# Kernel optimization log

Hardware: AMD Instinct MI355X
Metric: run time of the kernel (lower is better)

## Reference

```python
import jax, jax.numpy as jnp
import numpy as np

# Dimensions matching init_kwargs
O = 4096   # out_features
I = 4096   # in_features
R = 32     # svd_rank
G = 64     # n_groups
GS = I // G  # group_size = 64
NBITS = 4
NUM_BYTES = O * I * NBITS // 8


def setup_inputs() -> dict:
    key = jax.random.key(0)
    ks = jax.random.split(key, 7)
    return {
        "x": jax.random.normal(ks[0], (1, 4096, I), dtype=jnp.float32),
        # bit-packed int4 weights, two nibbles per byte (stored as int32 holding 0..255)
        "w_packed": jax.random.randint(ks[1], (NUM_BYTES,), 0, 256, dtype=jnp.int32),
        "svd_up": jax.random.normal(ks[2], (O, R), dtype=jnp.float32) * 0.02,
        "svd_down": jax.random.normal(ks[3], (R, I), dtype=jnp.float32) * 0.02,
        "scale": jax.random.uniform(ks[4], (O, G, 1), dtype=jnp.float32, minval=0.001, maxval=0.02),
        "zero_point": jax.random.uniform(ks[5], (O, G, 1), dtype=jnp.float32, minval=0.0, maxval=15.0),
        "bias": jax.random.normal(ks[6], (O,), dtype=jnp.float32) * 0.01,
    }


def _dequantize(w_packed, svd_up, svd_down, scale, zero_point):
    # Unpack two 4-bit values per byte (low nibble first).
    low = w_packed & 0xF
    high = (w_packed >> 4) & 0xF
    w_q = jnp.stack([low, high], axis=-1).reshape(O, G, GS).astype(jnp.float32)
    # Per-group affine dequant: (q - zero) * scale, then SVD low-rank correction.
    W = ((w_q - zero_point) * scale).reshape(O, I)
    return W + svd_up @ svd_down  # [O, I]


def reference(x, w_packed, svd_up, svd_down, scale, zero_point, bias):
    # forward_int8 path (tokens > 16, int8_matmul=True)
    W_f = _dequantize(w_packed, svd_up, svd_down, scale, zero_point).T  # [I, O]
    xm = x.reshape(-1, I)  # [N, I]
    # Dynamic per-row activation quant
    scale_x = jnp.max(jnp.abs(xm), axis=1, keepdims=True) / 127.0  # [N, 1]
    x_q = jnp.clip(jnp.round(xm / scale_x), -128, 127).astype(jnp.int8)
    # Dynamic per-column weight quant
    scale_w = jnp.max(jnp.abs(W_f), axis=0, keepdims=True) / 127.0  # [1, O]
    W_q = jnp.clip(jnp.round(W_f / scale_w), -128, 127).astype(jnp.int8)
    # int8 GEMM with int32 accumulation, then dequant scales + bias
    acc = jnp.matmul(x_q.astype(jnp.int32), W_q.astype(jnp.int32))  # [N, O] int32
    out = acc.astype(jnp.float32) * scale_x * scale_w + bias
    return out.reshape(*x.shape[:-1], O)
```

## Files before the change

### kernel.cpp

```cpp
#include <hip/hip_runtime.h>
#include <cstdint>
#include <cstddef>

#define I_DIM 4096
#define O_DIM 4096
#define RNK 32
#define NGRP 64
#define N_TOK 4096

typedef int v4i  __attribute__((ext_vector_type(4)));
typedef int v16i __attribute__((ext_vector_type(16)));

__device__ __forceinline__ int clamp_i8(float v) {
    int q = (int)rintf(v);
    q = q < -128 ? -128 : q;
    q = q > 127 ? 127 : q;
    return q;
}

#define BO 4

__global__ __launch_bounds__(256, 4) void quant_w_kernel(
    const int* __restrict__ w_packed, const float* __restrict__ svd_up,
    const float* __restrict__ svd_down, const float* __restrict__ scale,
    const float* __restrict__ zp, char* __restrict__ w_q,
    float* __restrict__ scale_w)
{
    __shared__ float s_sc[BO][NGRP];
    __shared__ float s_zp[BO][NGRP];
    __shared__ float s_red[BO][4];
    __shared__ float s_sw[BO];

    const int tid = threadIdx.x;
    const int o0 = blockIdx.x * BO;

    for (int t = tid; t < BO * NGRP; t += 256) {
        s_sc[t >> 6][t & 63] = scale[(size_t)(o0 + (t >> 6)) * NGRP + (t & 63)];
        s_zp[t >> 6][t & 63] = zp[(size_t)(o0 + (t >> 6)) * NGRP + (t & 63)];
    }
    __syncthreads();

    float W[4][BO][4];
    float vmax[BO];
#pragma unroll
    for (int ro = 0; ro < BO; ro++) vmax[ro] = 0.0f;

#pragma unroll
    for (int jq = 0; jq < 4; jq++) {
        const int q = tid + 256 * jq;
        const int i = 4 * q;
        const int g = q >> 4;

#pragma unroll
        for (int ro = 0; ro < BO; ro++) {
            const int2 b2 = *(const int2*)&w_packed[(size_t)(o0 + ro) * (I_DIM / 2) + 2 * q];
            const float sc = s_sc[ro][g], z = s_zp[ro][g];
            W[jq][ro][0] = ((float)(b2.x & 0xF) - z) * sc;
            W[jq][ro][1] = ((float)((b2.x >> 4) & 0xF) - z) * sc;
            W[jq][ro][2] = ((float)(b2.y & 0xF) - z) * sc;
            W[jq][ro][3] = ((float)((b2.y >> 4) & 0xF) - z) * sc;
        }

#pragma unroll 4
        for (int r = 0; r < RNK; r++) {
            const float4 d = *(const float4*)&svd_down[(size_t)r * I_DIM + i];
#pragma unroll
            for (int ro = 0; ro < BO; ro++) {
                const float u = svd_up[(size_t)(o0 + ro) * RNK + r];
                W[jq][ro][0] += u * d.x;
                W[jq][ro][1] += u * d.y;
                W[jq][ro][2] += u * d.z;
                W[jq][ro][3] += u * d.w;
            }
        }

#pragma unroll
        for (int ro = 0; ro < BO; ro++) {
            vmax[ro] = fmaxf(vmax[ro],
                fmaxf(fmaxf(fabsf(W[jq][ro][0]), fabsf(W[jq][ro][1])),
                      fmaxf(fabsf(W[jq][ro][2]), fabsf(W[jq][ro][3]))));
        }
    }

    const int lane = tid & 63, wv = tid >> 6;
#pragma unroll
    for (int ro = 0; ro < BO; ro++) {
        float m = vmax[ro];
        for (int off = 32; off > 0; off >>= 1)
            m = fmaxf(m, __shfl_down(m, off, 64));
        if (lane == 0) s_red[ro][wv] = m;
    }
    __syncthreads();
    if (tid < BO) {
        const float m = fmaxf(fmaxf(s_red[tid][0], s_red[tid][1]),
                              fmaxf(s_red[tid][2], s_red[tid][3]));
        const float sw = m / 127.0f;
        scale_w[o0 + tid] = sw;
        s_sw[tid] = sw;
    }
    __syncthreads();

    float inv[BO];
#pragma unroll
    for (int ro = 0; ro < BO; ro++) inv[ro] = 1.0f / s_sw[ro];

#pragma unroll
    for (int jq = 0; jq < 4; jq++) {
        const int q = tid + 256 * jq;
#pragma unroll
        for (int ro = 0; ro < BO; ro++) {
            const int q0 = clamp_i8(W[jq][ro][0] * inv[ro]);
            const int q1 = clamp_i8(W[jq][ro][1] * inv[ro]);
            const int q2 = clamp_i8(W[jq][ro][2] * inv[ro]);
            const int q3 = clamp_i8(W[jq][ro][3] * inv[ro]);
            ((int*)w_q)[(size_t)(o0 + ro) * (I_DIM / 4) + q] =
                (q0 & 0xFF) | ((q1 & 0xFF) << 8) | ((q2 & 0xFF) << 16) | ((q3 & 0xFF) << 24);
        }
    }
}

__global__ __launch_bounds__(256) void quant_x_kernel(
    const float* __restrict__ x, char* __restrict__ x_q,
    float* __restrict__ scale_x)
{
    const int n = blockIdx.x;
    const int tid = threadIdx.x;
    const float4* xr = (const float4*)(x + (size_t)n * I_DIM);
    float4 v[4];
    float m = 0.0f;
#pragma unroll
    for (int j = 0; j < 4; j++) {
        v[j] = xr[tid + 256 * j];
        m = fmaxf(m, fmaxf(fmaxf(fabsf(v[j].x), fabsf(v[j].y)),
                           fmaxf(fabsf(v[j].z), fabsf(v[j].w))));
    }
    __shared__ float s_red[4];
    __shared__ float s_sx;
    for (int off = 32; off > 0; off >>= 1)
        m = fmaxf(m, __shfl_down(m, off, 64));
    if ((tid & 63) == 0) s_red[tid >> 6] = m;
    __syncthreads();
    if (tid == 0) {
        const float mm = fmaxf(fmaxf(s_red[0], s_red[1]),
                               fmaxf(s_red[2], s_red[3]));
        const float sx = mm / 127.0f;
        scale_x[n] = sx;
        s_sx = sx;
    }
    __syncthreads();
    const float sx = s_sx;
    int* outw = (int*)(x_q + (size_t)n * I_DIM);
#pragma unroll
    for (int j = 0; j < 4; j++) {
        const int q0 = clamp_i8(v[j].x / sx);
        const int q1 = clamp_i8(v[j].y / sx);
        const int q2 = clamp_i8(v[j].z / sx);
        const int q3 = clamp_i8(v[j].w / sx);
        outw[tid + 256 * j] =
            (q0 & 0xFF) | ((q1 & 0xFF) << 8) | ((q2 & 0xFF) << 16) | ((q3 & 0xFF) << 24);
    }
}

#define BM 128
#define BN 128
#define BK 128

__global__ __launch_bounds__(256) void gemm_i8_kernel(
    const char* __restrict__ x_q, const char* __restrict__ w_q,
    const float* __restrict__ scale_x, const float* __restrict__ scale_w,
    const float* __restrict__ bias, float* __restrict__ out)
{
    __shared__ v4i As4[BM * BK / 16];
    __shared__ v4i Bs4[BN * BK / 16];
    char* As = (char*)As4;
    char* Bs = (char*)Bs4;

    const int tid = threadIdx.x;
    const int id = blockIdx.x;
    const int xcd = id & 7;
    const int s_lin = id >> 3;
    const int bm0 = (s_lin & 31) * BM;
    const int bn0 = (xcd * 4 + (s_lin >> 5)) * BN;

    const int lane = tid & 63, wv = tid >> 6;
    const int wm = wv & 1, wn = wv >> 1;
    const int l31 = lane & 31, h = lane >> 5;

    v16i acc[2][2];
#pragma unroll
    for (int mt = 0; mt < 2; mt++)
#pragma unroll
        for (int nt = 0; nt < 2; nt++)
            acc[mt][nt] = (v16i)(0);

    for (int kk = 0; kk < I_DIM / BK; kk++) {
        const int k0 = kk * BK;
#pragma unroll
        for (int j = 0; j < 4; j++) {
            const int c = tid + 256 * j;
            const int row = c >> 3;
            const int kc = (c & 7) ^ (row & 7);
            const char* ga = x_q + (size_t)(bm0 + row) * I_DIM + k0 + kc * 16;
            __builtin_amdgcn_global_load_lds(
                (const __attribute__((address_space(1))) unsigned int*)ga,
                (__attribute__((address_space(3))) unsigned int*)(As + c * 16),
                16, 0, 0);
            const char* gb = w_q + (size_t)(bn0 + row) * I_DIM + k0 + kc * 16;
            __builtin_amdgcn_global_load_lds(
                (const __attribute__((address_space(1))) unsigned int*)gb,
                (__attribute__((address_space(3))) unsigned int*)(Bs + c * 16),
                16, 0, 0);
        }
        __syncthreads();
#pragma unroll
        for (int s = 0; s < 4; s++) {
            v4i af[2], bf[2];
#pragma unroll
            for (int mt = 0; mt < 2; mt++) {
                const int row = wm * 64 + mt * 32 + l31;
                const int kc = (s * 2 + h) ^ (row & 7);
                af[mt] = *(const v4i*)(As + row * BK + kc * 16);
            }
#pragma unroll
            for (int nt = 0; nt < 2; nt++) {
                const int row = wn * 64 + nt * 32 + l31;
                const int kc = (s * 2 + h) ^ (row & 7);
                bf[nt] = *(const v4i*)(Bs + row * BK + kc * 16);
            }
#pragma unroll
            for (int mt = 0; mt < 2; mt++)
#pragma unroll
                for (int nt = 0; nt < 2; nt++)
                    acc[mt][nt] = __builtin_amdgcn_mfma_i32_32x32x32_i8(
                        af[mt], bf[nt], acc[mt][nt], 0, 0, 0);
        }
        __syncthreads();
    }

#pragma unroll
    for (int mt = 0; mt < 2; mt++) {
        const int rbase = bm0 + wm * 64 + mt * 32 + 4 * h;
        float sx[16];
#pragma unroll
        for (int reg = 0; reg < 16; reg++)
            sx[reg] = scale_x[rbase + (reg & 3) + 8 * (reg >> 2)];
#pragma unroll
        for (int nt = 0; nt < 2; nt++) {
            const int oc = bn0 + wn * 64 + nt * 32 + l31;
            const float sw = scale_w[oc];
            const float bs = bias[oc];
#pragma unroll
            for (int reg = 0; reg < 16; reg++) {
                const int rr = rbase + (reg & 3) + 8 * (reg >> 2);
                out[(size_t)rr * O_DIM + oc] =
                    (float)acc[mt][nt][reg] * sx[reg] * sw + bs;
            }
        }
    }
}

extern "C" void kernel_launch(void* const* d_in, const int* in_sizes, int n_in,
                              void* d_out, int out_size, void* d_ws, size_t ws_size,
                              hipStream_t stream) {
    const float* x        = (const float*)d_in[0];
    const int*   w_packed = (const int*)d_in[1];
    const float* svd_up   = (const float*)d_in[2];
    const float* svd_down = (const float*)d_in[3];
    const float* scale    = (const float*)d_in[4];
    const float* zp       = (const float*)d_in[5];
    const float* bias     = (const float*)d_in[6];
    float* out = (float*)d_out;

    char* ws = (char*)d_ws;
    char*  w_q     = ws;
    char*  x_q     = ws + ((size_t)16 << 20);
    float* scale_w = (float*)(ws + ((size_t)32 << 20));
    float* scale_x = (float*)(ws + ((size_t)32 << 20) + 16384);

    quant_w_kernel<<<O_DIM / BO, 256, 0, stream>>>(w_packed, svd_up, svd_down,
                                                   scale, zp, w_q, scale_w);
    quant_x_kernel<<<N_TOK, 256, 0, stream>>>(x, x_q, scale_x);
    gemm_i8_kernel<<<(N_TOK / BM) * (O_DIM / BN), 256, 0, stream>>>(
        x_q, w_q, scale_x, scale_w, bias, out);
}
```

Measured before the change: 261.3 us.

## Merge quant kernels and rewrite int8 GEMM with 256x256 triple-buffered pipeline

```diff
diff --git a/kernel.cpp b/kernel.cpp
--- a/kernel.cpp
+++ b/kernel.cpp
@@ -19,12 +19,13 @@
 }
 
 #define BO 4
-
-__global__ __launch_bounds__(256, 4) void quant_w_kernel(
+#define W_BLOCKS (O_DIM / BO)
+
+__device__ __forceinline__ void quant_w_body(
     const int* __restrict__ w_packed, const float* __restrict__ svd_up,
     const float* __restrict__ svd_down, const float* __restrict__ scale,
     const float* __restrict__ zp, char* __restrict__ w_q,
-    float* __restrict__ scale_w)
+    float* __restrict__ scale_w, int blk)
 {
     __shared__ float s_sc[BO][NGRP];
     __shared__ float s_zp[BO][NGRP];
@@ -32,7 +33,7 @@
     __shared__ float s_sw[BO];
 
     const int tid = threadIdx.x;
-    const int o0 = blockIdx.x * BO;
+    const int o0 = blk * BO;
 
     for (int t = tid; t < BO * NGRP; t += 256) {
         s_sc[t >> 6][t & 63] = scale[(size_t)(o0 + (t >> 6)) * NGRP + (t & 63)];
@@ -41,16 +42,11 @@
     __syncthreads();
 
     float W[4][BO][4];
-    float vmax[BO];
-#pragma unroll
-    for (int ro = 0; ro < BO; ro++) vmax[ro] = 0.0f;
 
 #pragma unroll
     for (int jq = 0; jq < 4; jq++) {
         const int q = tid + 256 * jq;
-        const int i = 4 * q;
         const int g = q >> 4;
-
 #pragma unroll
         for (int ro = 0; ro < BO; ro++) {
             const int2 b2 = *(const int2*)&w_packed[(size_t)(o0 + ro) * (I_DIM / 2) + 2 * q];
@@ -60,27 +56,39 @@
             W[jq][ro][2] = ((float)(b2.y & 0xF) - z) * sc;
             W[jq][ro][3] = ((float)((b2.y >> 4) & 0xF) - z) * sc;
         }
-
-#pragma unroll 4
-        for (int r = 0; r < RNK; r++) {
-            const float4 d = *(const float4*)&svd_down[(size_t)r * I_DIM + i];
+    }
+
+#pragma unroll 2
+    for (int r = 0; r < RNK; r++) {
+        float u[BO];
+#pragma unroll
+        for (int ro = 0; ro < BO; ro++)
+            u[ro] = svd_up[(size_t)(o0 + ro) * RNK + r];
+        float4 d[4];
+#pragma unroll
+        for (int jq = 0; jq < 4; jq++)
+            d[jq] = *(const float4*)&svd_down[(size_t)r * I_DIM + 4 * (tid + 256 * jq)];
+#pragma unroll
+        for (int jq = 0; jq < 4; jq++)
 #pragma unroll
             for (int ro = 0; ro < BO; ro++) {
-                const float u = svd_up[(size_t)(o0 + ro) * RNK + r];
-                W[jq][ro][0] += u * d.x;
-                W[jq][ro][1] += u * d.y;
-                W[jq][ro][2] += u * d.z;
-                W[jq][ro][3] += u * d.w;
+                W[jq][ro][0] += u[ro] * d[jq].x;
+                W[jq][ro][1] += u[ro] * d[jq].y;
+                W[jq][ro][2] += u[ro] * d[jq].z;
+                W[jq][ro][3] += u[ro] * d[jq].w;
             }
-        }
-
-#pragma unroll
-        for (int ro = 0; ro < BO; ro++) {
+    }
+
+    float vmax[BO];
+#pragma unroll
+    for (int ro = 0; ro < BO; ro++) vmax[ro] = 0.0f;
+#pragma unroll
+    for (int jq = 0; jq < 4; jq++)
+#pragma unroll
+        for (int ro = 0; ro < BO; ro++)
             vmax[ro] = fmaxf(vmax[ro],
                 fmaxf(fmaxf(fabsf(W[jq][ro][0]), fabsf(W[jq][ro][1])),
                       fmaxf(fabsf(W[jq][ro][2]), fabsf(W[jq][ro][3]))));
-        }
-    }
 
     const int lane = tid & 63, wv = tid >> 6;
 #pragma unroll
@@ -119,11 +127,10 @@
     }
 }
 
-__global__ __launch_bounds__(256) void quant_x_kernel(
+__device__ __forceinline__ void quant_x_body(
     const float* __restrict__ x, char* __restrict__ x_q,
-    float* __restrict__ scale_x)
-{
-    const int n = blockIdx.x;
+    float* __restrict__ scale_x, int n)
+{
     const int tid = threadIdx.x;
     const float4* xr = (const float4*)(x + (size_t)n * I_DIM);
     float4 v[4];
@@ -161,85 +168,128 @@
     }
 }
 
-#define BM 128
-#define BN 128
-#define BK 128
-
-__global__ __launch_bounds__(256) void gemm_i8_kernel(
+__global__ __launch_bounds__(256, 4) void prep_kernel(
+    const int* __restrict__ w_packed, const float* __restrict__ svd_up,
+    const float* __restrict__ svd_down, const float* __restrict__ scale,
+    const float* __restrict__ zp, char* __restrict__ w_q,
+    float* __restrict__ scale_w,
+    const float* __restrict__ x, char* __restrict__ x_q,
+    float* __restrict__ scale_x)
+{
+    if (blockIdx.x < W_BLOCKS)
+        quant_w_body(w_packed, svd_up, svd_down, scale, zp, w_q, scale_w, blockIdx.x);
+    else
+        quant_x_body(x, x_q, scale_x, blockIdx.x - W_BLOCKS);
+}
+
+#define TBM 256
+#define TBN 256
+#define TBK 64
+#define NKT (I_DIM / TBK)
+
+__device__ __forceinline__ void stage_tile(const char* __restrict__ src, int row0,
+                                           int t, char* lds_mat, int tid)
+{
+#pragma unroll
+    for (int uu = 0; uu < 2; uu++) {
+        const int c = tid + uu * 512;
+        const int row = c >> 2;
+        const int kc = (c & 3) ^ ((row >> 1) & 3);
+        const char* g = src + (size_t)(row0 + row) * I_DIM + t * TBK + kc * 16;
+        __builtin_amdgcn_global_load_lds(
+            (const __attribute__((address_space(1))) unsigned int*)g,
+            (__attribute__((address_space(3))) unsigned int*)(lds_mat + c * 16),
+            16, 0, 0);
+    }
+}
+
+#define READ_FRAGS(P) do {                                                  \
+    _Pragma("unroll")                                                       \
+    for (int mt = 0; mt < 4; mt++) {                                        \
+        const int row = wm * 128 + mt * 32 + l31;                           \
+        const int kc = ((P) * 2 + h) ^ ((row >> 1) & 3);                    \
+        af[mt] = *(const v4i*)(Ac + row * TBK + kc * 16);                   \
+    }                                                                       \
+    _Pragma("unroll")                                                       \
+    for (int nt = 0; nt < 2; nt++) {                                        \
+        const int row = wn * 64 + nt * 32 + l31;                            \
+        const int kc = ((P) * 2 + h) ^ ((row >> 1) & 3);                    \
+        bf[nt] = *(const v4i*)(Bc + row * TBK + kc * 16);                   \
+    }                                                                       \
+} while (0)
+
+#define MFMA_CLUSTER() do {                                                 \
+    __builtin_amdgcn_s_setprio(1);                                          \
+    _Pragma("unroll")                                                       \
+    for (int mt = 0; mt < 4; mt++)                                          \
+        _Pragma("unroll")                                                   \
+        for (int nt = 0; nt < 2; nt++)                                      \
+            acc[mt][nt] = __builtin_amdgcn_mfma_i32_32x32x32_i8(            \
+                af[mt], bf[nt], acc[mt][nt], 0, 0, 0);                      \
+    __builtin_amdgcn_s_setprio(0);                                          \
+} while (0)
+
+__global__ __launch_bounds__(512, 2) void gemm_i8_kernel(
     const char* __restrict__ x_q, const char* __restrict__ w_q,
     const float* __restrict__ scale_x, const float* __restrict__ scale_w,
     const float* __restrict__ bias, float* __restrict__ out)
 {
-    __shared__ v4i As4[BM * BK / 16];
-    __shared__ v4i Bs4[BN * BK / 16];
-    char* As = (char*)As4;
-    char* Bs = (char*)Bs4;
+    __shared__ v4i smem4[3 * 2 * 1024];
+    char* lds = (char*)smem4;
 
     const int tid = threadIdx.x;
     const int id = blockIdx.x;
     const int xcd = id & 7;
-    const int s_lin = id >> 3;
-    const int bm0 = (s_lin & 31) * BM;
-    const int bn0 = (xcd * 4 + (s_lin >> 5)) * BN;
+    const int s = id >> 3;
+    const int bm0 = (s & 15) * TBM;
+    const int bn0 = (xcd * 2 + (s >> 4)) * TBN;
 
     const int lane = tid & 63, wv = tid >> 6;
-    const int wm = wv & 1, wn = wv >> 1;
+    const int wm = wv >> 2, wn = wv & 3;
     const int l31 = lane & 31, h = lane >> 5;
 
-    v16i acc[2][2];
-#pragma unroll
-    for (int mt = 0; mt < 2; mt++)
+    v16i acc[4][2];
+#pragma unroll
+    for (int mt = 0; mt < 4; mt++)
 #pragma unroll
         for (int nt = 0; nt < 2; nt++)
             acc[mt][nt] = (v16i)(0);
 
-    for (int kk = 0; kk < I_DIM / BK; kk++) {
-        const int k0 = kk * BK;
-#pragma unroll
-        for (int j = 0; j < 4; j++) {
-            const int c = tid + 256 * j;
-            const int row = c >> 3;
-            const int kc = (c & 7) ^ (row & 7);
-            const char* ga = x_q + (size_t)(bm0 + row) * I_DIM + k0 + kc * 16;
-            __builtin_amdgcn_global_load_lds(
-                (const __attribute__((address_space(1))) unsigned int*)ga,
-                (__attribute__((address_space(3))) unsigned int*)(As + c * 16),
-                16, 0, 0);
-            const char* gb = w_q + (size_t)(bn0 + row) * I_DIM + k0 + kc * 16;
-            __builtin_amdgcn_global_load_lds(
-                (const __attribute__((address_space(1))) unsigned int*)gb,
-                (__attribute__((address_space(3))) unsigned int*)(Bs + c * 16),
-                16, 0, 0);
-        }
-        __syncthreads();
-#pragma unroll
-        for (int s = 0; s < 4; s++) {
-            v4i af[2], bf[2];
-#pragma unroll
-            for (int mt = 0; mt < 2; mt++) {
-                const int row = wm * 64 + mt * 32 + l31;
-                const int kc = (s * 2 + h) ^ (row & 7);
-                af[mt] = *(const v4i*)(As + row * BK + kc * 16);
-            }
-#pragma unroll
-            for (int nt = 0; nt < 2; nt++) {
-                const int row = wn * 64 + nt * 32 + l31;
-                const int kc = (s * 2 + h) ^ (row & 7);
-                bf[nt] = *(const v4i*)(Bs + row * BK + kc * 16);
-            }
-#pragma unroll
-            for (int mt = 0; mt < 2; mt++)
-#pragma unroll
-                for (int nt = 0; nt < 2; nt++)
-                    acc[mt][nt] = __builtin_amdgcn_mfma_i32_32x32x32_i8(
-                        af[mt], bf[nt], acc[mt][nt], 0, 0, 0);
-        }
-        __syncthreads();
-    }
-
-#pragma unroll
-    for (int mt = 0; mt < 2; mt++) {
-        const int rbase = bm0 + wm * 64 + mt * 32 + 4 * h;
+    stage_tile(x_q, bm0, 0, lds + 0 * 16384, tid);
+    stage_tile(w_q, bn0, 0, lds + 1 * 16384, tid);
+    stage_tile(x_q, bm0, 1, lds + 2 * 16384, tid);
+    stage_tile(w_q, bn0, 1, lds + 3 * 16384, tid);
+    asm volatile("s_waitcnt vmcnt(4)" ::: "memory");
+    __builtin_amdgcn_s_barrier();
+
+    int cb = 0, nb = 2;
+    for (int t = 0; t < NKT; ++t) {
+        char* Ac = lds + (2 * cb + 0) * 16384;
+        char* Bc = lds + (2 * cb + 1) * 16384;
+        const bool pf = (t + 2 < NKT);
+        v4i af[4], bf[2];
+
+        if (pf) stage_tile(x_q, bm0, t + 2, lds + (2 * nb + 0) * 16384, tid);
+        READ_FRAGS(0);
+        __builtin_amdgcn_s_barrier();
+        MFMA_CLUSTER();
+        __builtin_amdgcn_s_barrier();
+
+        if (pf) stage_tile(w_q, bn0, t + 2, lds + (2 * nb + 1) * 16384, tid);
+        READ_FRAGS(1);
+        __builtin_amdgcn_s_barrier();
+        MFMA_CLUSTER();
+        if (t < NKT - 2)       asm volatile("s_waitcnt vmcnt(4)" ::: "memory");
+        else if (t == NKT - 2) asm volatile("s_waitcnt vmcnt(0)" ::: "memory");
+        if (t < NKT - 1) __builtin_amdgcn_s_barrier();
+
+        cb = (cb == 2) ? 0 : cb + 1;
+        nb = (nb == 2) ? 0 : nb + 1;
+    }
+
+#pragma unroll
+    for (int mt = 0; mt < 4; mt++) {
+        const int rbase = bm0 + wm * 128 + mt * 32 + 4 * h;
         float sx[16];
 #pragma unroll
         for (int reg = 0; reg < 16; reg++)
@@ -277,9 +327,8 @@
     float* scale_w = (float*)(ws + ((size_t)32 << 20));
     float* scale_x = (float*)(ws + ((size_t)32 << 20) + 16384);
 
-    quant_w_kernel<<<O_DIM / BO, 256, 0, stream>>>(w_packed, svd_up, svd_down,
-                                                   scale, zp, w_q, scale_w);
-    quant_x_kernel<<<N_TOK, 256, 0, stream>>>(x, x_q, scale_x);
-    gemm_i8_kernel<<<(N_TOK / BM) * (O_DIM / BN), 256, 0, stream>>>(
+    prep_kernel<<<W_BLOCKS + N_TOK, 256, 0, stream>>>(
+        w_packed, svd_up, svd_down, scale, zp, w_q, scale_w, x, x_q, scale_x);
+    gemm_i8_kernel<<<(N_TOK / TBM) * (O_DIM / TBN), 512, 0, stream>>>(
         x_q, w_q, scale_x, scale_w, bias, out);
 }
```

Result: faster. 254.7 us (-2.5%).
